# Optimization experiments

Hardware: AMD Instinct MI355X
Metric: run time of the kernel (lower is better)

Reference implementation:

```python
import jax, jax.numpy as jnp
import numpy as np

TOKENS, D_MODEL, D_FF, RANK = 16384, 1024, 2816, 16


def setup_inputs() -> dict:
    key = jax.random.key(0)
    ks = jax.random.split(key, 7)
    s = lambda k, shp, scale: jax.random.normal(k, shp, dtype=jnp.float32) * scale
    return {
        "x": s(ks[0], (TOKENS, D_MODEL), 1.0),
        "W_gate_up": s(ks[1], (D_MODEL, 2 * D_FF), 0.02),
        "A_gate_up": s(ks[2], (D_MODEL, RANK), 0.02),
        "B_gate_up": s(ks[3], (RANK, 2 * D_FF), 0.02),
        "W_down": s(ks[4], (D_FF, D_MODEL), 0.02),
        "A_down": s(ks[5], (D_FF, RANK), 0.02),
        "B_down": s(ks[6], (RANK, D_MODEL), 0.02),
    }


def reference(x, W_gate_up, A_gate_up, B_gate_up, W_down, A_down, B_down):
    # gate_up_proj: base GEMM + LoRA low-rank correction
    gate_up = x @ W_gate_up + (x @ A_gate_up) @ B_gate_up  # [T, 2*D_FF]
    gate, up = jnp.split(gate_up, 2, axis=-1)
    h = jax.nn.silu(gate) * up  # SiluAndMul, [T, D_FF]
    # down_proj: base GEMM + LoRA correction
    out = h @ W_down + (h @ A_down) @ B_down  # [T, D_MODEL]
    return out
```

## Files before the change

kernel.cpp:

```cpp
#include <hip/hip_runtime.h>


typedef __bf16 bf16_t;
typedef __bf16 bf16x4 __attribute__((ext_vector_type(4)));
typedef __bf16 bf16x8 __attribute__((ext_vector_type(8)));
typedef float f32x4 __attribute__((ext_vector_type(4)));

#define TOKENS 16384
#define DMODEL 1024
#define DFF    2816
#define N2F    5632

#define BARM() asm volatile("s_barrier" ::: "memory")
#define VMW(n) asm volatile("s_waitcnt vmcnt(" #n ")" ::: "memory")
#define MFMA(d, va, vb) d = __builtin_amdgcn_mfma_f32_16x16x32_bf16(va, vb, d, 0, 0, 0)
#define LD8(p) (*(const bf16x8*)(p))
#define SGB(m, n) __builtin_amdgcn_sched_group_barrier(m, n, 0)
#define SGB_PATTERN() do {                                                        \
    SGB(0x010, 4);                                                                \
    SGB(0x100, 2); SGB(0x008, 5);                                                 \
    SGB(0x100, 2); SGB(0x008, 5);                                                 \
    SGB(0x100, 2); SGB(0x008, 5);                                                 \
    SGB(0x100, 2); SGB(0x008, 5);                                                 \
    SGB(0x100, 2); SGB(0x008, 6);                                                 \
    SGB(0x100, 2); SGB(0x008, 6); } while (0)

__device__ __forceinline__ void gload16(const bf16_t* g, bf16_t* l) {
    __builtin_amdgcn_global_load_lds(
        (const __attribute__((address_space(1))) void*)g,
        (__attribute__((address_space(3))) void*)l, 16, 0, 0);
}

template<int KTOT, int NTOT>
__device__ __forceinline__ void prep_body(
        const float* __restrict__ W, const float* __restrict__ A,
        const float* __restrict__ B, bf16_t* __restrict__ Wt,
        int k0, int n0, int t) {
    __shared__ float Ws[64][65];
    __shared__ float As[64][17];
    __shared__ float Bs[16][64];
    #pragma unroll
    for (int i = 0; i < 16; ++i) {
        int row = i * 4 + t / 64, col = t % 64;
        Ws[row][col] = W[(size_t)(k0 + row) * NTOT + n0 + col];
    }
    #pragma unroll
    for (int i = 0; i < 4; ++i) {
        int idx = i * 256 + t;
        As[idx / 16][idx % 16] = A[(size_t)(k0 + idx / 16) * 16 + idx % 16];
    }
    #pragma unroll
    for (int i = 0; i < 4; ++i) {
        int idx = i * 256 + t;
        Bs[idx / 64][idx % 64] = B[(size_t)(idx / 64) * NTOT + n0 + idx % 64];
    }
    __syncthreads();
    const int kl = t % 64;
    #pragma unroll
    for (int j = 0; j < 16; ++j) {
        int nl = j * 4 + t / 64;
        float val = Ws[kl][nl];
        #pragma unroll
        for (int r = 0; r < 16; ++r) val += As[kl][r] * Bs[r][nl];
        Wt[(size_t)(n0 + nl) * KTOT + k0 + kl] = (bf16_t)val;
    }
}

__global__ __launch_bounds__(256) void prologue(
        const float* __restrict__ x,
        const float* __restrict__ Wgu, const float* __restrict__ Agu,
        const float* __restrict__ Bgu,
        const float* __restrict__ Wd,  const float* __restrict__ Ad,
        const float* __restrict__ Bd,
        bf16_t* __restrict__ wgut, bf16_t* __restrict__ wdt,
        bf16_t* __restrict__ xb) {
    const int b = blockIdx.x, t = threadIdx.x;
    if (b < 1408) {
        prep_body<DMODEL, N2F>(Wgu, Agu, Bgu, wgut,
                               (b & 15) * 64, (b >> 4) * 64, t);
    } else if (b < 2112) {
        const int b2 = b - 1408;
        prep_body<DFF, DMODEL>(Wd, Ad, Bd, wdt,
                               (b2 % 44) * 64, (b2 / 44) * 64, t);
    } else {
        const int i = (b - 2112) * 256 + t;
        float4 v = ((const float4*)x)[i];
        bf16x4 o;
        o.x = (bf16_t)v.x; o.y = (bf16_t)v.y; o.z = (bf16_t)v.z; o.w = (bf16_t)v.w;
        ((bf16x4*)xb)[i] = o;
    }
}

__global__ __launch_bounds__(512, 2) void gemm1(
        const bf16_t* __restrict__ X, const bf16_t* __restrict__ Wt,
        bf16_t* __restrict__ H) {
    __shared__ bf16_t lds[65536];
    const int t = threadIdx.x, l = t & 63;
    const int wid = t >> 6, wr = wid >> 2, wc = wid & 3;
    const int l15 = l & 15, lhi = l >> 4;
    const int wgl = ((int)blockIdx.x & 7) * 176 + ((int)blockIdx.x >> 3);
    const int tf = wgl % 22, tm = wgl / 22;
    const int mbase = tm * 256, fbase = tf * 128;
    const int srow = t >> 2;
    const int sc8 = ((t & 3) ^ (srow & 3)) * 8;
    const bf16_t* gA  = X + (size_t)(mbase + srow) * DMODEL + sc8;
    const bf16_t* gA2 = gA + (size_t)128 * DMODEL;
    const bf16_t* gBg = Wt + (size_t)(fbase + srow) * DMODEL + sc8;
    const bf16_t* gBu = Wt + (size_t)(DFF + fbase + srow) * DMODEL + sc8;
    const int rsw = (lhi ^ (l15 & 3)) * 8;
    const int aoff = (wr * 128 + l15) * 32 + rsw;
    const int boff = 8192 + (wc * 32 + l15) * 32 + rsw;

    f32x4 accg[8][2] = {}, accu[8][2] = {};
    bf16x8 a0[8], g0[2], u0[2], a1[8], g1[2], u1[2];
    const int NT1 = DMODEL / 32;

#define G1_STAGE(kt) do { const int kc = (kt) * 32;                               \
    bf16_t* p = lds + (((kt) & 3) << 14) + wid * 512;                             \
    gload16(gA  + kc, p);                                                         \
    gload16(gA2 + kc, p + 4096);                                                  \
    gload16(gBg + kc, p + 8192);                                                  \
    gload16(gBu + kc, p + 12288); } while (0)
#define G1_READ(aa, gg, uu, bi) do {                                              \
    const bf16_t* _pa = lds + ((bi) << 14) + aoff;                                \
    aa[0] = LD8(_pa);        aa[1] = LD8(_pa + 512);                              \
    aa[2] = LD8(_pa + 1024); aa[3] = LD8(_pa + 1536);                             \
    aa[4] = LD8(_pa + 2048); aa[5] = LD8(_pa + 2560);                             \
    aa[6] = LD8(_pa + 3072); aa[7] = LD8(_pa + 3584);                             \
    const bf16_t* _pb = lds + ((bi) << 14) + boff;                                \
    gg[0] = LD8(_pb);        gg[1] = LD8(_pb + 512);                              \
    uu[0] = LD8(_pb + 4096); uu[1] = LD8(_pb + 4608); } while (0)
#define G1_MFMA(aa, gg, uu) do {                                                  \
    _Pragma("unroll")                                                             \
    for (int m = 0; m < 8; ++m) {                                                 \
        MFMA(accg[m][0], aa[m], gg[0]); MFMA(accu[m][0], aa[m], uu[0]);           \
        MFMA(accg[m][1], aa[m], gg[1]); MFMA(accu[m][1], aa[m], uu[1]);           \
    } } while (0)
#define G1_ITER(kt, aaU, ggU, uuU, aaR, ggR, uuR) do {                            \
    VMW(4); BARM();                                                               \
    if ((kt) + 3 < NT1) G1_STAGE((kt) + 3);                                       \
    G1_READ(aaR, ggR, uuR, ((kt) + 1) & 3);                                       \
    G1_MFMA(aaU, ggU, uuU);                                                       \
    SGB_PATTERN(); } while (0)

    G1_STAGE(0); G1_STAGE(1); G1_STAGE(2);
    VMW(8); BARM();
    G1_READ(a0, g0, u0, 0);
    for (int kt2 = 0; kt2 < NT1 - 2; kt2 += 2) {
        G1_ITER(kt2,     a0, g0, u0, a1, g1, u1);
        G1_ITER(kt2 + 1, a1, g1, u1, a0, g0, u0);
    }
    VMW(0); BARM();
    G1_READ(a1, g1, u1, (NT1 - 1) & 3);
    G1_MFMA(a0, g0, u0);
    G1_MFMA(a1, g1, u1);
#undef G1_ITER
#undef G1_STAGE
#undef G1_READ
#undef G1_MFMA

    #pragma unroll
    for (int m = 0; m < 8; ++m)
        #pragma unroll
        for (int n = 0; n < 2; ++n)
            #pragma unroll
            for (int r = 0; r < 4; ++r) {
                int row = mbase + wr * 128 + m * 16 + lhi * 4 + r;
                int col = fbase + wc * 32 + n * 16 + l15;
                float g = accg[m][n][r], u = accu[m][n][r];
                H[(size_t)row * DFF + col] = (bf16_t)(g / (1.0f + __expf(-g)) * u);
            }
}

__global__ __launch_bounds__(512, 2) void gemm2(
        const bf16_t* __restrict__ Hm, const bf16_t* __restrict__ Wt,
        float* __restrict__ O) {
    __shared__ bf16_t lds[65536];
    const int t = threadIdx.x, l = t & 63;
    const int wid = t >> 6, wr = wid >> 2, wc = wid & 3;
    const int l15 = l & 15, lhi = l >> 4;
    const int wgl = ((int)blockIdx.x & 7) * 32 + ((int)blockIdx.x >> 3);
    const int tn = wgl % 4, tm = wgl / 4;
    const int mbase = tm * 256, nbase = tn * 256;
    const int srow = t >> 2;
    const int sc8 = ((t & 3) ^ (srow & 3)) * 8;
    const bf16_t* gA  = Hm + (size_t)(mbase + srow) * DFF + sc8;
    const bf16_t* gA2 = gA + (size_t)128 * DFF;
    const bf16_t* gB  = Wt + (size_t)(nbase + srow) * DFF + sc8;
    const bf16_t* gB2 = gB + (size_t)128 * DFF;
    const int rsw = (lhi ^ (l15 & 3)) * 8;
    const int aoff = (wr * 128 + l15) * 32 + rsw;
    const int boff = 8192 + (wc * 64 + l15) * 32 + rsw;

    f32x4 acc[8][4] = {};
    bf16x8 a0[8], b0[4], a1[8], b1[4];
    const int NT2 = DFF / 32;

#define G2_STAGE(kt) do { const int kc = (kt) * 32;                               \
    bf16_t* p = lds + (((kt) & 3) << 14) + wid * 512;                             \
    gload16(gA  + kc, p);                                                         \
    gload16(gA2 + kc, p + 4096);                                                  \
    gload16(gB  + kc, p + 8192);                                                  \
    gload16(gB2 + kc, p + 12288); } while (0)
#define G2_READ(aa, bb, bi) do {                                                  \
    const bf16_t* _pa = lds + ((bi) << 14) + aoff;                                \
    aa[0] = LD8(_pa);        aa[1] = LD8(_pa + 512);                              \
    aa[2] = LD8(_pa + 1024); aa[3] = LD8(_pa + 1536);                             \
    aa[4] = LD8(_pa + 2048); aa[5] = LD8(_pa + 2560);                             \
    aa[6] = LD8(_pa + 3072); aa[7] = LD8(_pa + 3584);                             \
    const bf16_t* _pb = lds + ((bi) << 14) + boff;                                \
    bb[0] = LD8(_pb);        bb[1] = LD8(_pb + 512);                              \
    bb[2] = LD8(_pb + 1024); bb[3] = LD8(_pb + 1536); } while (0)
#define G2_MFMA(aa, bb) do {                                                      \
    _Pragma("unroll")                                                             \
    for (int m = 0; m < 8; ++m) {                                                 \
        MFMA(acc[m][0], aa[m], bb[0]); MFMA(acc[m][1], aa[m], bb[1]);             \
        MFMA(acc[m][2], aa[m], bb[2]); MFMA(acc[m][3], aa[m], bb[3]);             \
    } } while (0)
#define G2_ITER(kt, aaU, bbU, aaR, bbR) do {                                      \
    VMW(4); BARM();                                                               \
    if ((kt) + 3 < NT2) G2_STAGE((kt) + 3);                                       \
    G2_READ(aaR, bbR, ((kt) + 1) & 3);                                            \
    G2_MFMA(aaU, bbU);                                                            \
    SGB_PATTERN(); } while (0)

    G2_STAGE(0); G2_STAGE(1); G2_STAGE(2);
    VMW(8); BARM();
    G2_READ(a0, b0, 0);
    for (int kt2 = 0; kt2 < NT2 - 2; kt2 += 2) {
        G2_ITER(kt2,     a0, b0, a1, b1);
        G2_ITER(kt2 + 1, a1, b1, a0, b0);
    }
    VMW(0); BARM();
    G2_READ(a1, b1, (NT2 - 1) & 3);
    G2_MFMA(a0, b0);
    G2_MFMA(a1, b1);
#undef G2_STAGE
#undef G2_READ
#undef G2_MFMA
#undef G2_ITER

    #pragma unroll
    for (int m = 0; m < 8; ++m)
        #pragma unroll
        for (int n = 0; n < 4; ++n)
            #pragma unroll
            for (int r = 0; r < 4; ++r) {
                int row = mbase + wr * 128 + m * 16 + lhi * 4 + r;
                int col = nbase + wc * 64 + n * 16 + l15;
                O[(size_t)row * DMODEL + col] = acc[m][n][r];
            }
}

extern "C" void kernel_launch(void* const* d_in, const int* in_sizes, int n_in,
                              void* d_out, int out_size, void* d_ws, size_t ws_size,
                              hipStream_t stream) {
    const float* x   = (const float*)d_in[0];
    const float* Wgu = (const float*)d_in[1];
    const float* Agu = (const float*)d_in[2];
    const float* Bgu = (const float*)d_in[3];
    const float* Wd  = (const float*)d_in[4];
    const float* Ad  = (const float*)d_in[5];
    const float* Bd  = (const float*)d_in[6];
    float* out = (float*)d_out;
    char* ws = (char*)d_ws;

    bf16_t* wgut = (bf16_t*)(ws);
    bf16_t* wdt  = (bf16_t*)(ws + 11534336);
    bf16_t* xb   = (bf16_t*)(ws + 17301504);
    bf16_t* hb   = (bf16_t*)(ws + 50855936);

    prologue<<<18496, 256, 0, stream>>>(x, Wgu, Agu, Bgu, Wd, Ad, Bd,
                                        wgut, wdt, xb);
    gemm1<<<22 * 64, 512, 0, stream>>>(xb, wgut, hb);
    gemm2<<<8 * 32, 512, 0, stream>>>(hb, wdt, out);
}
```

Baseline: 317.7 us.

## Restructure down-proj GEMM pipeline to stage two K-tiles per barrier

The second GEMM's K loop now issues global-to-LDS loads for two tiles at once and synchronizes once per pair of tiles with a full vmcnt(0) wait, instead of waiting per tile with a partial vmcnt. A new scheduling pattern interleaves 8 loads with LDS reads and MFMAs across the doubled body. This halves barrier count but drains all outstanding loads at each barrier, reducing prefetch depth and possibly exposing memory latency.

```diff
diff --git a/kernel.cpp b/kernel.cpp
--- a/kernel.cpp
+++ b/kernel.cpp
@@ -24,6 +24,20 @@
     SGB(0x100, 2); SGB(0x008, 5);                                                 \
     SGB(0x100, 2); SGB(0x008, 6);                                                 \
     SGB(0x100, 2); SGB(0x008, 6); } while (0)
+#define SGB_PATTERN2() do {                                                       \
+    SGB(0x010, 8);                                                                \
+    SGB(0x100, 2); SGB(0x008, 5);                                                 \
+    SGB(0x100, 2); SGB(0x008, 5);                                                 \
+    SGB(0x100, 2); SGB(0x008, 5);                                                 \
+    SGB(0x100, 2); SGB(0x008, 5);                                                 \
+    SGB(0x100, 2); SGB(0x008, 5);                                                 \
+    SGB(0x100, 2); SGB(0x008, 5);                                                 \
+    SGB(0x100, 2); SGB(0x008, 5);                                                 \
+    SGB(0x100, 2); SGB(0x008, 5);                                                 \
+    SGB(0x100, 2); SGB(0x008, 5);                                                 \
+    SGB(0x100, 2); SGB(0x008, 5);                                                 \
+    SGB(0x100, 2); SGB(0x008, 7);                                                 \
+    SGB(0x100, 2); SGB(0x008, 7); } while (0)
 
 __device__ __forceinline__ void gload16(const bf16_t* g, bf16_t* l) {
     __builtin_amdgcn_global_load_lds(
@@ -217,28 +231,26 @@
         MFMA(acc[m][0], aa[m], bb[0]); MFMA(acc[m][1], aa[m], bb[1]);             \
         MFMA(acc[m][2], aa[m], bb[2]); MFMA(acc[m][3], aa[m], bb[3]);             \
     } } while (0)
-#define G2_ITER(kt, aaU, bbU, aaR, bbR) do {                                      \
-    VMW(4); BARM();                                                               \
-    if ((kt) + 3 < NT2) G2_STAGE((kt) + 3);                                       \
-    G2_READ(aaR, bbR, ((kt) + 1) & 3);                                            \
-    G2_MFMA(aaU, bbU);                                                            \
-    SGB_PATTERN(); } while (0)
-
-    G2_STAGE(0); G2_STAGE(1); G2_STAGE(2);
-    VMW(8); BARM();
+
+    G2_STAGE(0); G2_STAGE(1);
+    VMW(0); BARM();
+    G2_STAGE(2); G2_STAGE(3);
     G2_READ(a0, b0, 0);
-    for (int kt2 = 0; kt2 < NT2 - 2; kt2 += 2) {
-        G2_ITER(kt2,     a0, b0, a1, b1);
-        G2_ITER(kt2 + 1, a1, b1, a0, b0);
-    }
-    VMW(0); BARM();
-    G2_READ(a1, b1, (NT2 - 1) & 3);
+    G2_READ(a1, b1, 1);
     G2_MFMA(a0, b0);
+    for (int s2 = 2; s2 <= NT2 - 2; s2 += 2) {
+        VMW(0); BARM();
+        if (s2 + 2 < NT2) { G2_STAGE(s2 + 2); G2_STAGE(s2 + 3); }
+        G2_READ(a0, b0, s2 & 3);
+        G2_MFMA(a1, b1);
+        G2_READ(a1, b1, (s2 + 1) & 3);
+        G2_MFMA(a0, b0);
+        SGB_PATTERN2();
+    }
     G2_MFMA(a1, b1);
 #undef G2_STAGE
 #undef G2_READ
 #undef G2_MFMA
-#undef G2_ITER
 
     #pragma unroll
     for (int m = 0; m < 8; ++m)
```

Result: no change. 322.2 us (+1.4%).
